# Performance work log

Measured on AMD Instinct MI355X. Metric: run time of the kernel, lower is better.

Reference implementation:

```python
import jax, jax.numpy as jnp
import numpy as np

N_HEADS = 16
D_K = 64
DIM = 1024
NEG = -1e12
LN_EPS = 1e-5


def setup_inputs() -> dict:
    key = jax.random.key(0)
    ks = jax.random.split(key, 8)
    B, S, D = 2, 2048, DIM
    H, K = N_HEADS, D_K
    f = lambda k, shp: jax.random.normal(k, shp, dtype=jnp.float32)
    scale = 0.02
    return {
        "input_Q": f(ks[0], (B, S, D)),
        "input_K": f(ks[1], (B, S, D)),
        "input_V": f(ks[2], (B, S, D)),
        "attention_mask": jax.random.randint(ks[3], (B, S), 0, 2, dtype=jnp.int32),
        "W_Q": f(ks[4], (H * K, D)) * scale,  # nn.Linear weight layout [out, in]
        "W_K": f(ks[5], (H * K, D)) * scale,
        "W_V": f(ks[6], (H * K, D)) * scale,
        "W_O": f(ks[7], (D, H * K)) * scale,
        "gamma": jnp.ones((D,), jnp.float32),
        "beta": jnp.zeros((D,), jnp.float32),
    }


def reference(input_Q, input_K, input_V, attention_mask, W_Q, W_K, W_V, W_O, gamma, beta):
    B, S, D = input_Q.shape

    def proj(x, W):  # [B,S,D] @ [HK,D]^T -> [B,H,S,K]
        return (x @ W.T).reshape(B, S, N_HEADS, D_K).transpose(0, 2, 1, 3)

    Q = proj(input_Q, W_Q)
    K = proj(input_K, W_K)
    V = proj(input_V, W_V)

    scores = jnp.einsum('bhqk,bhsk->bhqs', Q, K) / np.float32(np.sqrt(D_K))

    # Faithful reproduction of scores_mask (including its inverted-looking logic):
    # mask = clamp(padding_mask + strict_upper_tri - 1, min=0); scores += (1-mask)*NEG
    am = attention_mask.astype(scores.dtype)[:, None, None, :]          # [B,1,1,S]
    low_tri = jnp.triu(jnp.ones((S, S), scores.dtype), k=1)             # 1 - tril(ones)
    m = jnp.maximum(am + low_tri - 1.0, 0.0)
    scores = scores + (1.0 - m) * NEG

    attn = jax.nn.softmax(scores, axis=-1)
    ctx = jnp.einsum('bhqs,bhsk->bhqk', attn, V)                        # [B,H,S,K]
    ctx = ctx.transpose(0, 2, 1, 3).reshape(B, S, N_HEADS * D_K)

    out = ctx @ W_O.T + input_Q                                         # fc + residual
    mu = jnp.mean(out, axis=-1, keepdims=True)
    var = jnp.var(out, axis=-1, keepdims=True)
    return (out - mu) / jnp.sqrt(var + LN_EPS) * gamma + beta
```

## Files before the change

kernel.cpp:

```cpp
#include <hip/hip_runtime.h>

#define NH    16
#define DK    64
#define DIM   1024
#define BATCH 2
#define SEQ   2048
#define MROWS (BATCH*SEQ)
#define QSCALE 0.18033688011112043f
#define SENT   -44.0f
#define PCONST 5.684341886080802e-14f

typedef unsigned short bfraw;
typedef __attribute__((ext_vector_type(8))) __bf16 bf16x8;
typedef __attribute__((ext_vector_type(4))) __bf16 bf16x4;
typedef __attribute__((ext_vector_type(8))) unsigned short u16x8;
typedef __attribute__((ext_vector_type(4))) unsigned short u16x4;
typedef __attribute__((ext_vector_type(4))) short s16x4;
typedef __attribute__((ext_vector_type(4))) float f32x4;

__device__ __forceinline__ float bf2f(bfraw u) {
    union { unsigned int i; float f; } x; x.i = ((unsigned int)u) << 16; return x.f;
}
__device__ __forceinline__ bfraw f2bf(float f) {
    union { float f; unsigned int i; } x; x.f = f;
    unsigned int r = x.i + 0x7FFFu + ((x.i >> 16) & 1u);
    return (bfraw)(r >> 16);
}
__device__ __forceinline__ float fexp2(float x) {
#if __has_builtin(__builtin_amdgcn_exp2f)
    return __builtin_amdgcn_exp2f(x);
#else
    return exp2f(x);
#endif
}

__device__ __forceinline__ f32x4 mfma16(s16x4 a, s16x4 b, f32x4 c) {
#if __has_builtin(__builtin_amdgcn_mfma_f32_16x16x16_bf16)
    union { s16x4 s; bf16x4 h; } ua, ub; ua.s = a; ub.s = b;
    return __builtin_amdgcn_mfma_f32_16x16x16_bf16(ua.h, ub.h, c, 0, 0, 0);
#elif __has_builtin(__builtin_amdgcn_mfma_f32_16x16x16bf16_1k)
    return __builtin_amdgcn_mfma_f32_16x16x16bf16_1k(a, b, c, 0, 0, 0);
#else
    asm("v_mfma_f32_16x16x16_bf16 %0, %1, %2, %0" : "+v"(c) : "v"(a), "v"(b));
    return c;
#endif
}

__device__ __forceinline__ float block_reduce(float val, float* rbuf, int op) {
    const int lane = threadIdx.x & 63, wave = threadIdx.x >> 6;
    #pragma unroll
    for (int off = 32; off; off >>= 1) {
        float o = __shfl_xor(val, off, 64);
        val = op ? (val + o) : fmaxf(val, o);
    }
    if (lane == 0) rbuf[wave] = val;
    __syncthreads();
    float r = op ? (rbuf[0] + rbuf[1] + rbuf[2] + rbuf[3])
                 : fmaxf(fmaxf(rbuf[0], rbuf[1]), fmaxf(rbuf[2], rbuf[3]));
    __syncthreads();
    return r;
}

__global__ __launch_bounds__(256) void cvt_kernel(
        const float* __restrict__ x0, const float* __restrict__ x1, const float* __restrict__ x2,
        const float* __restrict__ w0, const float* __restrict__ w1, const float* __restrict__ w2,
        const float* __restrict__ w3, bfraw* __restrict__ Xb, bfraw* __restrict__ Wb) {
    const int t = blockIdx.y;
    const float* src; bfraw* dst; int n;
    if (t < 3) { src = (t == 0) ? x0 : (t == 1) ? x1 : x2; dst = Xb + t * (MROWS * DIM); n = MROWS * DIM; }
    else { int u = t - 3; src = (u == 0) ? w0 : (u == 1) ? w1 : (u == 2) ? w2 : w3;
           dst = Wb + u * (DIM * DIM); n = DIM * DIM; }
    int idx = (blockIdx.x * 256 + threadIdx.x) * 8;
    if (idx >= n) return;
    f32x4 a = *(const f32x4*)(src + idx);
    f32x4 b = *(const f32x4*)(src + idx + 4);
    u16x8 o;
    #pragma unroll
    for (int j = 0; j < 4; j++) { o[j] = f2bf(a[j]); o[4 + j] = f2bf(b[j]); }
    *(u16x8*)(dst + idx) = o;
}

__device__ __forceinline__ void gemm128(const bfraw* __restrict__ A, const bfraw* __restrict__ B,
                                        int m0, int n0, f32x4 acc[4][4]) {
    __shared__ __align__(16) bfraw As[2][128 * 64];
    __shared__ __align__(16) bfraw Bs[2][128 * 64];
    const int tid = threadIdx.x, wave = tid >> 6;
    const int lane = tid & 63, lrow = lane & 15, quad = lane >> 4;
    const int wy = wave >> 1, wx = wave & 1;
    const int swz = lrow & 7;
    const int srow = tid >> 2;
    const int cg0  = (tid & 3) << 1;
    const int gc   = cg0 << 3;
    const int e7   = srow & 7;
    const int o0 = ((cg0 ^ e7) << 3), o1 = (((cg0 | 1) ^ e7) << 3);

    const bfraw* pa0 = A + (m0 + srow) * DIM + gc;
    const bfraw* pa1 = A + (m0 + 64 + srow) * DIM + gc;
    const bfraw* pb0 = B + (n0 + srow) * DIM + gc;
    const bfraw* pb1 = B + (n0 + 64 + srow) * DIM + gc;

    #pragma unroll
    for (int i = 0; i < 4; i++)
        #pragma unroll
        for (int j = 0; j < 4; j++) { f32x4 z = {0.f, 0.f, 0.f, 0.f}; acc[i][j] = z; }

    u16x8 ha0[4], hb0[4], ha1[4], hb1[4];

    auto LOAD = [&](u16x8 ha[4], u16x8 hb[4], int kk) {
        ha[0] = *(const u16x8*)(pa0 + kk);     ha[1] = *(const u16x8*)(pa0 + kk + 8);
        ha[2] = *(const u16x8*)(pa1 + kk);     ha[3] = *(const u16x8*)(pa1 + kk + 8);
        hb[0] = *(const u16x8*)(pb0 + kk);     hb[1] = *(const u16x8*)(pb0 + kk + 8);
        hb[2] = *(const u16x8*)(pb1 + kk);     hb[3] = *(const u16x8*)(pb1 + kk + 8);
    };
    auto STORE = [&](bfraw* Ad, bfraw* Bd, u16x8 ha[4], u16x8 hb[4]) {
        *(u16x8*)&Ad[srow * 64 + o0]        = ha[0];
        *(u16x8*)&Ad[srow * 64 + o1]        = ha[1];
        *(u16x8*)&Ad[(64 + srow) * 64 + o0] = ha[2];
        *(u16x8*)&Ad[(64 + srow) * 64 + o1] = ha[3];
        *(u16x8*)&Bd[srow * 64 + o0]        = hb[0];
        *(u16x8*)&Bd[srow * 64 + o1]        = hb[1];
        *(u16x8*)&Bd[(64 + srow) * 64 + o0] = hb[2];
        *(u16x8*)&Bd[(64 + srow) * 64 + o1] = hb[3];
    };
    auto COMPUTE = [&](const bfraw* Ad, const bfraw* Bd) {
        #pragma unroll
        for (int ks = 0; ks < 2; ks++) {
            const int c = (ks << 2) | quad;
            bf16x8 af[4], bfg[4];
            #pragma unroll
            for (int mi = 0; mi < 4; mi++)
                af[mi] = *(const bf16x8*)&Ad[(wy * 64 + mi * 16 + lrow) * 64 + ((c ^ swz) << 3)];
            #pragma unroll
            for (int ni = 0; ni < 4; ni++)
                bfg[ni] = *(const bf16x8*)&Bd[(wx * 64 + ni * 16 + lrow) * 64 + ((c ^ swz) << 3)];
            #pragma unroll
            for (int mi = 0; mi < 4; mi++)
                #pragma unroll
                for (int ni = 0; ni < 4; ni++)
                    acc[mi][ni] = __builtin_amdgcn_mfma_f32_16x16x32_bf16(af[mi], bfg[ni], acc[mi][ni], 0, 0, 0);
        }
    };

    LOAD(ha0, hb0, 0);
    LOAD(ha1, hb1, 64);

    #pragma unroll
    for (int m2 = 0; m2 < DIM / 128; m2++) {
        const int k0 = m2 * 128;
        STORE(As[0], Bs[0], ha0, hb0);
        if (k0 + 128 < DIM) LOAD(ha0, hb0, k0 + 128);
        __syncthreads();
        COMPUTE(As[0], Bs[0]);
        STORE(As[1], Bs[1], ha1, hb1);
        if (k0 + 192 < DIM) LOAD(ha1, hb1, k0 + 192);
        __syncthreads();
        COMPUTE(As[1], Bs[1]);
    }
}

__global__ __launch_bounds__(256) void qkv_gemm(
        const bfraw* __restrict__ Xb, const bfraw* __restrict__ Wb,
        bfraw* __restrict__ Qp, bfraw* __restrict__ Kp, bfraw* __restrict__ Vt) {
    const int which = blockIdx.z;
    const bfraw* A = Xb + which * (MROWS * DIM);
    const bfraw* B = Wb + which * (DIM * DIM);
    bfraw* O = (which == 0) ? Qp : (which == 1) ? Kp : Vt;
    const int m0 = blockIdx.x * 128, n0 = blockIdx.y * 128;
    f32x4 acc[4][4];
    gemm128(A, B, m0, n0, acc);
    const int lane = threadIdx.x & 63, wave = threadIdx.x >> 6;
    const int lrow = lane & 15, quad = lane >> 4;
    const int wy = wave >> 1, wx = wave & 1;
    const float scale = (which == 0) ? QSCALE : 1.0f;
    #pragma unroll
    for (int mi = 0; mi < 4; mi++)
        #pragma unroll
        for (int ni = 0; ni < 4; ni++)
            #pragma unroll
            for (int i = 0; i < 4; i++) {
                int m = m0 + wy * 64 + mi * 16 + quad * 4 + i;
                int n = n0 + wx * 64 + ni * 16 + lrow;
                int b = m >> 11, s = m & (SEQ - 1), h = n >> 6, kk = n & (DK - 1);
                bfraw v = f2bf(acc[mi][ni][i] * scale);
                if (which == 2) O[(((b * NH + h) * DK) + kk) * SEQ + s] = v;
                else            O[(((b * NH + h) * SEQ) + s) * DK + kk] = v;
            }
}

__global__ __launch_bounds__(256) void vsum_kernel(const bfraw* __restrict__ Vt,
                                                   float* __restrict__ Scum) {
    __shared__ float Ts[32][65];
    const int bh = blockIdx.x, tid = threadIdx.x;
    const int d = tid & 63, part = tid >> 6;
    const bfraw* vrow = Vt + (bh * DK + d) * SEQ;
    for (int qt = part * 8; qt < part * 8 + 8; qt++) {
        float s = 0.f;
        #pragma unroll
        for (int j = 0; j < 64; j += 8) {
            u16x8 v = *(const u16x8*)(vrow + qt * 64 + j);
            #pragma unroll
            for (int e = 0; e < 8; e++) s += bf2f(v[e]);
        }
        Ts[qt][d] = s;
    }
    __syncthreads();
    if (tid < 64) {
        float run = 0.f;
        for (int qt = 0; qt < 32; qt++) {
            Scum[(bh * 32 + qt) * 64 + tid] = run;
            run += Ts[qt][tid];
        }
    }
}

template<bool NEAR>
__device__ __forceinline__ void qk_soft(
        const bfraw* Kb, const bf16x8 qf[2], const float* Mkf,
        int kt0, int lrow, int quad, int q_ln, float& lsum, s16x4 pb[4]) {
    #pragma unroll
    for (int n = 0; n < 4; n++) {
        const int srow = n * 16 + lrow;
        bf16x8 kfa = *(const bf16x8*)&Kb[srow * 64 + ((quad ^ (lrow & 7)) << 3)];
        bf16x8 kfb = *(const bf16x8*)&Kb[srow * 64 + (((4 | quad) ^ (lrow & 7)) << 3)];
        f32x4 z = {0.f, 0.f, 0.f, 0.f};
        z = __builtin_amdgcn_mfma_f32_16x16x32_bf16(kfa, qf[0], z, 0, 0, 0);
        z = __builtin_amdgcn_mfma_f32_16x16x32_bf16(kfb, qf[1], z, 0, 0, 0);
        f32x4 mv = *(const f32x4*)&Mkf[kt0 + n * 16 + quad * 4];
        union { bf16x4 h; s16x4 s; } pk;
        #pragma unroll
        for (int i = 0; i < 4; i++) {
            float m = mv[i];
            if (NEAR) { int s = kt0 + n * 16 + quad * 4 + i; m = (s > q_ln) ? m : 0.0f; }
            float p = fexp2(fmaf(m, z[i] - SENT, SENT));
            lsum += p;
            pk.h[i] = (__bf16)p;
        }
        pb[n] = pk.s;
    }
}

__global__ __launch_bounds__(512) void attn_flash(
        const bfraw* __restrict__ Qp, const bfraw* __restrict__ Kp, const bfraw* __restrict__ Vt,
        const float* __restrict__ Scum, const int* __restrict__ mask, bfraw* __restrict__ Ctx) {
    __shared__ __align__(16) bfraw Ks[2][64 * 64];
    __shared__ __align__(16) bfraw Vs[2][64 * 64];
    __shared__ float Mkf[SEQ];
    const int bh = blockIdx.x, yy = blockIdx.y;
    const int gg = yy >> 3, jj = yy & 7;
    const int qt = gg ? (15 - jj) : jj;
    const int b = bh >> 4, h = bh & 15;
    const int tid = threadIdx.x, wave = tid >> 6, lane = tid & 63;
    const int lrow = lane & 15, quad = lane >> 4;
    const int baseK = ((b * NH + h) * SEQ) * DK;
    const int baseV = ((b * NH + h) * DK) * SEQ;
    const int qbase = qt * 128 + wave * 16;
    const int q_ln  = qbase + lrow;
    const int diagKt = qt * 128;
    const int ldr = tid >> 3;
    const int c8  = tid & 7;
    const int ldc = c8 << 3;
    const int cl  = ((c8 ^ (ldr & 7)) << 3);

    for (int i = tid; i < SEQ; i += 512) Mkf[i] = (mask[b * SEQ + i] != 0) ? 1.0f : 0.0f;

    bf16x8 qf[2];
    qf[0] = *(const bf16x8*)(Qp + baseK + q_ln * DK + quad * 8);
    qf[1] = *(const bf16x8*)(Qp + baseK + q_ln * DK + 32 + quad * 8);

    f32x4 Oa[4];
    const int scb = (bh * 32 + 2 * qt) * 64;
    #pragma unroll
    for (int nd = 0; nd < 4; nd++) {
        f32x4 sv = *(const f32x4*)&Scum[scb + nd * 16 + quad * 4];
        #pragma unroll
        for (int i = 0; i < 4; i++) Oa[nd][i] = PCONST * sv[i];
    }
    float lsum = 0.f;

    const int nt = (SEQ - diagKt) >> 6;
    int kt0 = diagKt;
    u16x8 k0 = *(const u16x8*)(Kp + baseK + (kt0 + ldr) * DK + ldc);
    u16x8 v0 = *(const u16x8*)(Vt + baseV + ldr * SEQ + kt0 + ldc);

    for (int t = 0; t < nt; t++, kt0 += 64) {
        bfraw* Kb = Ks[t & 1];
        bfraw* Vb = Vs[t & 1];
        *(u16x8*)&Kb[ldr * 64 + cl] = k0;
        *(u16x8*)&Vb[ldr * 64 + cl] = v0;
        if (t + 1 < nt) {
            const int kn = kt0 + 64;
            k0 = *(const u16x8*)(Kp + baseK + (kn + ldr) * DK + ldc);
            v0 = *(const u16x8*)(Vt + baseV + ldr * SEQ + kn + ldc);
        }
        __syncthreads();

        s16x4 pb[4];
        if (t < 2) qk_soft<true >(Kb, qf, Mkf, kt0, lrow, quad, q_ln, lsum, pb);
        else       qk_soft<false>(Kb, qf, Mkf, kt0, lrow, quad, q_ln, lsum, pb);

        #pragma unroll
        for (int nd = 0; nd < 4; nd++) {
            const int d = nd * 16 + lrow;
            #pragma unroll
            for (int sc = 0; sc < 4; sc++) {
                s16x4 vf = *(const s16x4*)&Vb[d * 64
                    + ((((sc << 1) | (quad >> 1)) ^ (d & 7)) << 3) + ((quad & 1) << 2)];
                Oa[nd] = mfma16(vf, pb[sc], Oa[nd]);
            }
        }
    }

    float r = lsum;
    r += __shfl_xor(r, 16, 64);
    r += __shfl_xor(r, 32, 64);
    const float inv = 1.0f / (r + (float)diagKt * PCONST);
    #pragma unroll
    for (int nd = 0; nd < 4; nd++) {
        u16x4 o;
        #pragma unroll
        for (int i = 0; i < 4; i++) o[i] = f2bf(Oa[nd][i] * inv);
        *(u16x4*)&Ctx[(b * SEQ + q_ln) * DIM + h * DK + nd * 16 + quad * 4] = o;
    }
}

__global__ __launch_bounds__(256) void out_gemm(
        const bfraw* __restrict__ Ctx, const bfraw* __restrict__ WoB, float* __restrict__ C) {
    const int m0 = blockIdx.x * 128, n0 = blockIdx.y * 128;
    f32x4 acc[4][4];
    gemm128(Ctx, WoB, m0, n0, acc);
    const int lane = threadIdx.x & 63, wave = threadIdx.x >> 6;
    const int lrow = lane & 15, quad = lane >> 4;
    const int wy = wave >> 1, wx = wave & 1;
    #pragma unroll
    for (int mi = 0; mi < 4; mi++)
        #pragma unroll
        for (int ni = 0; ni < 4; ni++)
            #pragma unroll
            for (int i = 0; i < 4; i++) {
                int m = m0 + wy * 64 + mi * 16 + quad * 4 + i;
                int n = n0 + wx * 64 + ni * 16 + lrow;
                C[m * DIM + n] = acc[mi][ni][i];
            }
}

__global__ __launch_bounds__(256) void ln_kernel(
        const float* __restrict__ C, const float* __restrict__ Xq,
        const float* __restrict__ gamma, const float* __restrict__ beta,
        float* __restrict__ out) {
    __shared__ float rbuf[4];
    const int m = blockIdx.x, tid = threadIdx.x;
    const float* crow = C + m * DIM;
    const float* xrow = Xq + m * DIM;
    float v[4]; float s = 0.f, s2 = 0.f;
    #pragma unroll
    for (int i = 0; i < 4; i++) {
        int d = tid + (i << 8);
        float x = crow[d] + xrow[d];
        v[i] = x; s += x; s2 += x * x;
    }
    float S  = block_reduce(s,  rbuf, 1);
    float S2 = block_reduce(s2, rbuf, 1);
    float mu  = S * (1.0f / DIM);
    float var = S2 * (1.0f / DIM) - mu * mu;
    float rstd = rsqrtf(var + 1e-5f);
    #pragma unroll
    for (int i = 0; i < 4; i++) {
        int d = tid + (i << 8);
        out[m * DIM + d] = (v[i] - mu) * rstd * gamma[d] + beta[d];
    }
}

extern "C" void kernel_launch(void* const* d_in, const int* in_sizes, int n_in,
                              void* d_out, int out_size, void* d_ws, size_t ws_size,
                              hipStream_t stream) {
    const float* Xq    = (const float*)d_in[0];
    const float* Xk    = (const float*)d_in[1];
    const float* Xv    = (const float*)d_in[2];
    const int*   mask  = (const int*)  d_in[3];
    const float* Wq    = (const float*)d_in[4];
    const float* Wk    = (const float*)d_in[5];
    const float* Wv    = (const float*)d_in[6];
    const float* Wo    = (const float*)d_in[7];
    const float* gamma = (const float*)d_in[8];
    const float* beta  = (const float*)d_in[9];
    float* out = (float*)d_out;

    char* ws = (char*)d_ws;
    bfraw* Xb   = (bfraw*)(ws);
    bfraw* Wb   = (bfraw*)(ws + (24u << 20));
    bfraw* Qp   = (bfraw*)(ws + (32u << 20));
    bfraw* Kp   = (bfraw*)(ws + (40u << 20));
    bfraw* Vt   = (bfraw*)(ws + (48u << 20));
    bfraw* Ctx  = (bfraw*)(ws + (56u << 20));
    float* C    = (float*)(ws);
    float* Scum = (float*)(ws + (16u << 20));

    dim3 blk(256);
    cvt_kernel<<<dim3(MROWS * DIM / (256 * 8), 7), blk, 0, stream>>>(Xq, Xk, Xv, Wq, Wk, Wv, Wo, Xb, Wb);
    qkv_gemm  <<<dim3(MROWS / 128, DIM / 128, 3),  blk, 0, stream>>>(Xb, Wb, Qp, Kp, Vt);
    vsum_kernel<<<dim3(BATCH * NH),                blk, 0, stream>>>(Vt, Scum);
    attn_flash<<<dim3(BATCH * NH, SEQ / 128),      dim3(512), 0, stream>>>(Qp, Kp, Vt, Scum, mask, Ctx);
    out_gemm  <<<dim3(MROWS / 128, DIM / 128),     blk, 0, stream>>>(Ctx, Wb + 3 * (DIM * DIM), C);
    ln_kernel <<<dim3(MROWS),                      blk, 0, stream>>>(C, Xq, gamma, beta, out);
}
```

Baseline: 219.2 us.

## Fold V prefix sums into attention and fuse LayerNorm into output GEMM

Removes the separate vsum kernel: each attention block now sums the V rows before its diagonal tile itself, reducing across waves in shared memory. It also removes the standalone LayerNorm kernel. The last of the 8 column blocks for each 128-row stripe, found with an atomic counter and threadfences, applies residual plus LayerNorm to those rows. This cuts two launches and their inter-kernel gaps, at the cost of redundant V reads in the attention kernel and a serialized LayerNorm tail in the final block of each stripe.

New measurement: 272.3 us. 1.24x slower.

```diff
diff --git a/kernel.cpp b/kernel.cpp
--- a/kernel.cpp
+++ b/kernel.cpp
@@ -44,21 +44,6 @@
     asm("v_mfma_f32_16x16x16_bf16 %0, %1, %2, %0" : "+v"(c) : "v"(a), "v"(b));
     return c;
 #endif
-}
-
-__device__ __forceinline__ float block_reduce(float val, float* rbuf, int op) {
-    const int lane = threadIdx.x & 63, wave = threadIdx.x >> 6;
-    #pragma unroll
-    for (int off = 32; off; off >>= 1) {
-        float o = __shfl_xor(val, off, 64);
-        val = op ? (val + o) : fmaxf(val, o);
-    }
-    if (lane == 0) rbuf[wave] = val;
-    __syncthreads();
-    float r = op ? (rbuf[0] + rbuf[1] + rbuf[2] + rbuf[3])
-                 : fmaxf(fmaxf(rbuf[0], rbuf[1]), fmaxf(rbuf[2], rbuf[3]));
-    __syncthreads();
-    return r;
 }
 
 __global__ __launch_bounds__(256) void cvt_kernel(
@@ -160,7 +145,10 @@
 
 __global__ __launch_bounds__(256) void qkv_gemm(
         const bfraw* __restrict__ Xb, const bfraw* __restrict__ Wb,
-        bfraw* __restrict__ Qp, bfraw* __restrict__ Kp, bfraw* __restrict__ Vt) {
+        bfraw* __restrict__ Qp, bfraw* __restrict__ Kp, bfraw* __restrict__ Vt,
+        int* __restrict__ cnt) {
+    if (blockIdx.x == 0 && blockIdx.y == 0 && blockIdx.z == 0 && threadIdx.x < 32)
+        cnt[threadIdx.x] = 0;
     const int which = blockIdx.z;
     const bfraw* A = Xb + which * (MROWS * DIM);
     const bfraw* B = Wb + which * (DIM * DIM);
@@ -187,32 +175,6 @@
             }
 }
 
-__global__ __launch_bounds__(256) void vsum_kernel(const bfraw* __restrict__ Vt,
-                                                   float* __restrict__ Scum) {
-    __shared__ float Ts[32][65];
-    const int bh = blockIdx.x, tid = threadIdx.x;
-    const int d = tid & 63, part = tid >> 6;
-    const bfraw* vrow = Vt + (bh * DK + d) * SEQ;
-    for (int qt = part * 8; qt < part * 8 + 8; qt++) {
-        float s = 0.f;
-        #pragma unroll
-        for (int j = 0; j < 64; j += 8) {
-            u16x8 v = *(const u16x8*)(vrow + qt * 64 + j);
-            #pragma unroll
-            for (int e = 0; e < 8; e++) s += bf2f(v[e]);
-        }
-        Ts[qt][d] = s;
-    }
-    __syncthreads();
-    if (tid < 64) {
-        float run = 0.f;
-        for (int qt = 0; qt < 32; qt++) {
-            Scum[(bh * 32 + qt) * 64 + tid] = run;
-            run += Ts[qt][tid];
-        }
-    }
-}
-
 template<bool NEAR>
 __device__ __forceinline__ void qk_soft(
         const bfraw* Kb, const bf16x8 qf[2], const float* Mkf,
@@ -241,10 +203,12 @@
 
 __global__ __launch_bounds__(512) void attn_flash(
         const bfraw* __restrict__ Qp, const bfraw* __restrict__ Kp, const bfraw* __restrict__ Vt,
-        const float* __restrict__ Scum, const int* __restrict__ mask, bfraw* __restrict__ Ctx) {
+        const int* __restrict__ mask, bfraw* __restrict__ Ctx) {
     __shared__ __align__(16) bfraw Ks[2][64 * 64];
     __shared__ __align__(16) bfraw Vs[2][64 * 64];
     __shared__ float Mkf[SEQ];
+    __shared__ float Ps[8][64];
+    __shared__ float Scol[64];
     const int bh = blockIdx.x, yy = blockIdx.y;
     const int gg = yy >> 3, jj = yy & 7;
     const int qt = gg ? (15 - jj) : jj;
@@ -261,20 +225,37 @@
     const int ldc = c8 << 3;
     const int cl  = ((c8 ^ (ldr & 7)) << 3);
 
+    const int d_v = tid & 63, part = tid >> 6;
+    float pacc = 0.f;
+    {
+        const bfraw* vrow = Vt + baseV + d_v * SEQ;
+        for (int s0 = part * 8; s0 < diagKt; s0 += 64) {
+            u16x8 v = *(const u16x8*)(vrow + s0);
+            #pragma unroll
+            for (int e = 0; e < 8; e++) pacc += bf2f(v[e]);
+        }
+    }
     for (int i = tid; i < SEQ; i += 512) Mkf[i] = (mask[b * SEQ + i] != 0) ? 1.0f : 0.0f;
+    Ps[part][d_v] = pacc;
+    __syncthreads();
+    if (tid < 64) {
+        float sc = 0.f;
+        #pragma unroll
+        for (int p = 0; p < 8; p++) sc += Ps[p][tid];
+        Scol[tid] = sc;
+    }
+    __syncthreads();
 
     bf16x8 qf[2];
     qf[0] = *(const bf16x8*)(Qp + baseK + q_ln * DK + quad * 8);
     qf[1] = *(const bf16x8*)(Qp + baseK + q_ln * DK + 32 + quad * 8);
 
     f32x4 Oa[4];
-    const int scb = (bh * 32 + 2 * qt) * 64;
-    #pragma unroll
-    for (int nd = 0; nd < 4; nd++) {
-        f32x4 sv = *(const f32x4*)&Scum[scb + nd * 16 + quad * 4];
-        #pragma unroll
-        for (int i = 0; i < 4; i++) Oa[nd][i] = PCONST * sv[i];
-    }
+    #pragma unroll
+    for (int nd = 0; nd < 4; nd++)
+        #pragma unroll
+        for (int i = 0; i < 4; i++)
+            Oa[nd][i] = PCONST * Scol[nd * 16 + quad * 4 + i];
     float lsum = 0.f;
 
     const int nt = (SEQ - diagKt) >> 6;
@@ -324,11 +305,15 @@
 }
 
 __global__ __launch_bounds__(256) void out_gemm(
-        const bfraw* __restrict__ Ctx, const bfraw* __restrict__ WoB, float* __restrict__ C) {
+        const bfraw* __restrict__ Ctx, const bfraw* __restrict__ WoB,
+        const float* __restrict__ Xq, const float* __restrict__ gamma,
+        const float* __restrict__ beta, float* __restrict__ C,
+        float* __restrict__ out, int* __restrict__ cnt) {
     const int m0 = blockIdx.x * 128, n0 = blockIdx.y * 128;
     f32x4 acc[4][4];
     gemm128(Ctx, WoB, m0, n0, acc);
-    const int lane = threadIdx.x & 63, wave = threadIdx.x >> 6;
+    const int tid = threadIdx.x;
+    const int lane = tid & 63, wave = tid >> 6;
     const int lrow = lane & 15, quad = lane >> 4;
     const int wy = wave >> 1, wx = wave & 1;
     #pragma unroll
@@ -341,32 +326,51 @@
                 int n = n0 + wx * 64 + ni * 16 + lrow;
                 C[m * DIM + n] = acc[mi][ni][i];
             }
-}
-
-__global__ __launch_bounds__(256) void ln_kernel(
-        const float* __restrict__ C, const float* __restrict__ Xq,
-        const float* __restrict__ gamma, const float* __restrict__ beta,
-        float* __restrict__ out) {
-    __shared__ float rbuf[4];
-    const int m = blockIdx.x, tid = threadIdx.x;
-    const float* crow = C + m * DIM;
-    const float* xrow = Xq + m * DIM;
-    float v[4]; float s = 0.f, s2 = 0.f;
-    #pragma unroll
-    for (int i = 0; i < 4; i++) {
-        int d = tid + (i << 8);
-        float x = crow[d] + xrow[d];
-        v[i] = x; s += x; s2 += x * x;
-    }
-    float S  = block_reduce(s,  rbuf, 1);
-    float S2 = block_reduce(s2, rbuf, 1);
-    float mu  = S * (1.0f / DIM);
-    float var = S2 * (1.0f / DIM) - mu * mu;
-    float rstd = rsqrtf(var + 1e-5f);
-    #pragma unroll
-    for (int i = 0; i < 4; i++) {
-        int d = tid + (i << 8);
-        out[m * DIM + d] = (v[i] - mu) * rstd * gamma[d] + beta[d];
+    __threadfence();
+    __syncthreads();
+    __shared__ int lastblk;
+    if (tid == 0) lastblk = (atomicAdd(&cnt[blockIdx.x], 1) == 7);
+    __syncthreads();
+    if (!lastblk) return;
+    __threadfence();
+
+    f32x4 g[4], bt[4];
+    #pragma unroll
+    for (int jj = 0; jj < 4; jj++) {
+        g[jj]  = *(const f32x4*)&gamma[lane * 16 + jj * 4];
+        bt[jj] = *(const f32x4*)&beta [lane * 16 + jj * 4];
+    }
+    for (int r = 0; r < 32; r++) {
+        const int row = m0 + wave + (r << 2);
+        const float* crow = C  + row * DIM + lane * 16;
+        const float* xrow = Xq + row * DIM + lane * 16;
+        f32x4 v[4]; float s = 0.f, s2 = 0.f;
+        #pragma unroll
+        for (int jj = 0; jj < 4; jj++) {
+            f32x4 cv = *(const f32x4*)(crow + jj * 4);
+            f32x4 xv = *(const f32x4*)(xrow + jj * 4);
+            #pragma unroll
+            for (int e = 0; e < 4; e++) {
+                float x = cv[e] + xv[e];
+                v[jj][e] = x; s += x; s2 += x * x;
+            }
+        }
+        #pragma unroll
+        for (int off = 1; off < 64; off <<= 1) {
+            s  += __shfl_xor(s,  off, 64);
+            s2 += __shfl_xor(s2, off, 64);
+        }
+        float mu   = s * (1.0f / DIM);
+        float var  = s2 * (1.0f / DIM) - mu * mu;
+        float rstd = rsqrtf(var + 1e-5f);
+        float* orow = out + row * DIM + lane * 16;
+        #pragma unroll
+        for (int jj = 0; jj < 4; jj++) {
+            f32x4 o;
+            #pragma unroll
+            for (int e = 0; e < 4; e++) o[e] = (v[jj][e] - mu) * rstd * g[jj][e] + bt[jj][e];
+            *(f32x4*)(orow + jj * 4) = o;
+        }
     }
 }
 
@@ -393,13 +397,11 @@
     bfraw* Vt   = (bfraw*)(ws + (48u << 20));
     bfraw* Ctx  = (bfraw*)(ws + (56u << 20));
     float* C    = (float*)(ws);
-    float* Scum = (float*)(ws + (16u << 20));
+    int*   cnt  = (int*)(ws + (16u << 20));
 
     dim3 blk(256);
     cvt_kernel<<<dim3(MROWS * DIM / (256 * 8), 7), blk, 0, stream>>>(Xq, Xk, Xv, Wq, Wk, Wv, Wo, Xb, Wb);
-    qkv_gemm  <<<dim3(MROWS / 128, DIM / 128, 3),  blk, 0, stream>>>(Xb, Wb, Qp, Kp, Vt);
-    vsum_kernel<<<dim3(BATCH * NH),                blk, 0, stream>>>(Vt, Scum);
-    attn_flash<<<dim3(BATCH * NH, SEQ / 128),      dim3(512), 0, stream>>>(Qp, Kp, Vt, Scum, mask, Ctx);
-    out_gemm  <<<dim3(MROWS / 128, DIM / 128),     blk, 0, stream>>>(Ctx, Wb + 3 * (DIM * DIM), C);
-    ln_kernel <<<dim3(MROWS),                      blk, 0, stream>>>(C, Xq, gamma, beta, out);
-}
+    qkv_gemm  <<<dim3(MROWS / 128, DIM / 128, 3),  blk, 0, stream>>>(Xb, Wb, Qp, Kp, Vt, cnt);
+    attn_flash<<<dim3(BATCH * NH, SEQ / 128),      dim3(512), 0, stream>>>(Qp, Kp, Vt, mask, Ctx);
+    out_gemm  <<<dim3(MROWS / 128, DIM / 128),     blk, 0, stream>>>(Ctx, Wb + 3 * (DIM * DIM), Xq, gamma, beta, C, out, cnt);
+}
```
